# Performance work log

Hardware: AMD Instinct MI355X
Metric: run time of the kernel (lower is better)

Reference implementation:

```python
import jax, jax.numpy as jnp
import numpy as np
import math

B, N, D, H, NBT = 16, 512, 512, 8, 5
HD = D // H
EPS = 1e-5

def _ln(x, g, b):
    mu = jnp.mean(x, axis=-1, keepdims=True)
    var = jnp.mean(jnp.square(x - mu), axis=-1, keepdims=True)
    return (x - mu) * jax.lax.rsqrt(var + EPS) * g + b

def setup_inputs() -> dict:
    key = jax.random.key(0)
    ks = jax.random.split(key, 16)
    s = 0.02
    inp = {
        'x': jax.random.normal(ks[0], (B, N, D), jnp.float32),
        'adj': jax.random.randint(ks[1], (B, N, N), 0, NBT, jnp.int64),
        'mask': (jax.random.uniform(ks[2], (B, N)) > 0.1).astype(jnp.float32),
        'Wq': jax.random.normal(ks[3], (D, D), jnp.float32) * s,
        'bq': jnp.zeros((D,), jnp.float32),
        'Wk': jax.random.normal(ks[4], (D, D), jnp.float32) * s,
        'bk': jnp.zeros((D,), jnp.float32),
        'Wv': jax.random.normal(ks[5], (D, D), jnp.float32) * s,
        'bv': jnp.zeros((D,), jnp.float32),
        'Wo': jax.random.normal(ks[6], (D, D), jnp.float32) * s,
        'bo': jnp.zeros((D,), jnp.float32),
        'edge_bias': jax.random.normal(ks[7], (NBT, H), jnp.float32) * s,
        'W1': jax.random.normal(ks[8], (D, 4 * D), jnp.float32) * s,
        'b1': jnp.zeros((4 * D,), jnp.float32),
        'W2': jax.random.normal(ks[9], (4 * D, D), jnp.float32) * s,
        'b2': jnp.zeros((D,), jnp.float32),
        'g1': jnp.ones((D,), jnp.float32),
        'beta1': jnp.zeros((D,), jnp.float32),
        'g2': jnp.ones((D,), jnp.float32),
        'beta2': jnp.zeros((D,), jnp.float32),
    }
    return inp

def reference(x, adj, mask, Wq, bq, Wk, bk, Wv, bv, Wo, bo, edge_bias,
              W1, b1, W2, b2, g1, beta1, g2, beta2):
    # --- attention block ---
    residual = x
    h = _ln(x, g1, beta1)
    # (B,N,D) -> (B,H,N,HD)
    Q = (h @ Wq + bq).reshape(B, N, H, HD).transpose(0, 2, 1, 3)
    K = (h @ Wk + bk).reshape(B, N, H, HD).transpose(0, 2, 1, 3)
    V = (h @ Wv + bv).reshape(B, N, H, HD).transpose(0, 2, 1, 3)
    attn = jnp.einsum('bhqd,bhkd->bhqk', Q, K) / math.sqrt(HD)
    # per-head edge-type bias: gather (B,N,N,H) -> (B,H,N,N)
    eb = edge_bias[adj].transpose(0, 3, 1, 2)
    attn = attn + eb
    mask_2d = mask[:, None, None, :] * mask[:, None, :, None]  # (B,1,N,N)
    attn = jnp.where(mask_2d == 0, -jnp.inf, attn)
    attn = jax.nn.softmax(attn, axis=-1)
    attn = jnp.nan_to_num(attn, nan=0.0)  # fully-masked rows -> 0
    out = jnp.einsum('bhqk,bhkd->bhqd', attn, V)
    out = out.transpose(0, 2, 1, 3).reshape(B, N, D)
    out = out @ Wo + bo
    x = residual + out  # dropout is identity in eval
    # --- FFN block ---
    residual = x
    h = _ln(x, g2, beta2)
    h = jax.nn.gelu(h @ W1 + b1, approximate=False) @ W2 + b2
    x = residual + h
    return x * mask[:, :, None]
```

## Files before the change

kernel.cpp:

```cpp
#include <hip/hip_runtime.h>
#include <hip/hip_bf16.h>
#include <math.h>
#include <stdint.h>

typedef __hip_bfloat16 bf16;
typedef __bf16 bf16x8 __attribute__((ext_vector_type(8)));
typedef float f32x4 __attribute__((ext_vector_type(4)));

#define MFMA16 __builtin_amdgcn_mfma_f32_16x16x32_bf16

__device__ __forceinline__ void gll16(const void* gsrc, void* ldst) {
  __builtin_amdgcn_global_load_lds(
      (const __attribute__((address_space(1))) unsigned int*)(uintptr_t)gsrc,
      (__attribute__((address_space(3))) unsigned int*)(uintptr_t)ldst,
      16, 0, 0);
}

__global__ __launch_bounds__(256) void pack_adj(const int* __restrict__ adj,
                                                const float* __restrict__ mask,
                                                unsigned char* __restrict__ out) {
  size_t i0 = ((size_t)blockIdx.x * 256 + threadIdx.x) * 16;
  int b = (int)(i0 >> 18);
  int k0 = (int)(i0 & 511);
  const float* mb = mask + b * 512 + k0;
  const int* ap = adj + i0;
  unsigned char o16[16];
#pragma unroll
  for (int j = 0; j < 16; ++j) {
    o16[j] = (unsigned char)(ap[j] | (mb[j] == 0.f ? 0x80 : 0));
  }
  *(uint4*)(out + i0) = *(const uint4*)o16;
}

__global__ __launch_bounds__(256) void transpose_wt6(
    const float* __restrict__ s0, const float* __restrict__ s1,
    const float* __restrict__ s2, const float* __restrict__ s3,
    const float* __restrict__ s4, const float* __restrict__ s5,
    bf16* __restrict__ d0, bf16* __restrict__ d1, bf16* __restrict__ d2,
    bf16* __restrict__ d3, bf16* __restrict__ d4, bf16* __restrict__ d5) {
  __shared__ float t[32][33];
  const int bid = blockIdx.x;
  const float* W;
  bf16* Wt;
  int K, N, n0, k0;
  if (bid < 1024) {
    int mi = bid >> 8, tt = bid & 255;
    W = (mi == 0) ? s0 : (mi == 1) ? s1 : (mi == 2) ? s2 : s3;
    Wt = (mi == 0) ? d0 : (mi == 1) ? d1 : (mi == 2) ? d2 : d3;
    K = 512; N = 512; n0 = (tt & 15) * 32; k0 = (tt >> 4) * 32;
  } else if (bid < 2048) {
    int tt = bid - 1024;
    W = s4; Wt = d4; K = 512; N = 2048;
    n0 = (tt & 63) * 32; k0 = (tt >> 6) * 32;
  } else {
    int tt = bid - 2048;
    W = s5; Wt = d5; K = 2048; N = 512;
    n0 = (tt & 15) * 32; k0 = (tt >> 4) * 32;
  }
  int tx = threadIdx.x, ty = threadIdx.y;
#pragma unroll
  for (int s = 0; s < 32; s += 8) t[ty + s][tx] = W[(size_t)(k0 + ty + s) * N + n0 + tx];
  __syncthreads();
#pragma unroll
  for (int s = 0; s < 32; s += 8) Wt[(size_t)(n0 + ty + s) * K + k0 + tx] = (bf16)t[tx][ty + s];
}

__global__ __launch_bounds__(256) void ln_k(const float* __restrict__ x,
                                            const float* __restrict__ gam,
                                            const float* __restrict__ bet,
                                            bf16* __restrict__ out) {
  int l = threadIdx.x & 63, w = threadIdx.x >> 6;
  size_t row = (size_t)blockIdx.x * 4 + w;
  const float* xr = x + row * 512 + l * 8;
  float4 v0 = *(const float4*)xr;
  float4 v1 = *(const float4*)(xr + 4);
  float s = v0.x + v0.y + v0.z + v0.w + v1.x + v1.y + v1.z + v1.w;
  float q = v0.x * v0.x + v0.y * v0.y + v0.z * v0.z + v0.w * v0.w +
            v1.x * v1.x + v1.y * v1.y + v1.z * v1.z + v1.w * v1.w;
#pragma unroll
  for (int o = 1; o < 64; o <<= 1) { s += __shfl_xor(s, o); q += __shfl_xor(q, o); }
  float mean = s * (1.0f / 512.0f);
  float var = q * (1.0f / 512.0f) - mean * mean;
  float rstd = rsqrtf(var + 1e-5f);
  const float* gr = gam + l * 8;
  const float* br = bet + l * 8;
  float4 ga = *(const float4*)gr, gb = *(const float4*)(gr + 4);
  float4 ba = *(const float4*)br, bb = *(const float4*)(br + 4);
  bf16 t8[8];
  t8[0] = (bf16)((v0.x - mean) * rstd * ga.x + ba.x);
  t8[1] = (bf16)((v0.y - mean) * rstd * ga.y + ba.y);
  t8[2] = (bf16)((v0.z - mean) * rstd * ga.z + ba.z);
  t8[3] = (bf16)((v0.w - mean) * rstd * ga.w + ba.w);
  t8[4] = (bf16)((v1.x - mean) * rstd * gb.x + bb.x);
  t8[5] = (bf16)((v1.y - mean) * rstd * gb.y + bb.y);
  t8[6] = (bf16)((v1.z - mean) * rstd * gb.z + bb.z);
  t8[7] = (bf16)((v1.w - mean) * rstd * gb.w + bb.w);
  *(uint4*)(out + row * 512 + l * 8) = *(const uint4*)t8;
}

template <int MODE, int BM, int BN>
__global__ __launch_bounds__(256) void gemm_bt(
    const bf16* __restrict__ A, const bf16* __restrict__ Bt, int M, int N, int K,
    const float* __restrict__ b0, const float* __restrict__ b1p,
    const float* __restrict__ b2p, const float* __restrict__ resid,
    const float* __restrict__ mrow, float* __restrict__ outF,
    bf16* __restrict__ outH) {
  constexpr int RA = BM / 32, RB = BN / 32;
  __shared__ __align__(16) bf16 Asw[2][BM * 64];
  __shared__ __align__(16) bf16 Bsw[2][BN * 64];
  const int tid = threadIdx.x;
  const int l = tid & 63, w = tid >> 6;
  const int g = l >> 4, ln = l & 15;
  const int wm = w >> 1, wn = w & 1;
  const int m0 = blockIdx.x * BM, n0 = blockIdx.y * BN;

  f32x4 acc[RA][RB];
  f32x4 zero = {0.f, 0.f, 0.f, 0.f};
#pragma unroll
  for (int i = 0; i < RA; ++i)
#pragma unroll
    for (int j = 0; j < RB; ++j) acc[i][j] = zero;

  const bf16* aSrc[RA];
  const bf16* bSrc[RB];
#pragma unroll
  for (int rr = 0; rr < RA; ++rr) {
    int m = w * (BM / 4) + rr * 8 + (l >> 3);
    int gs = (l & 7) ^ (m & 7);
    aSrc[rr] = A + (size_t)(m0 + m) * K + gs * 8;
  }
#pragma unroll
  for (int rr = 0; rr < RB; ++rr) {
    int n = w * (BN / 4) + rr * 8 + (l >> 3);
    int gs = (l & 7) ^ (n & 7);
    bSrc[rr] = Bt + (size_t)(n0 + n) * K + gs * 8;
  }

  const int NT = K >> 6;
#pragma unroll
  for (int rr = 0; rr < RA; ++rr) gll16(aSrc[rr], &Asw[0][w * (BM * 16) + rr * 512]);
#pragma unroll
  for (int rr = 0; rr < RB; ++rr) gll16(bSrc[rr], &Bsw[0][w * (BN * 16) + rr * 512]);
  __syncthreads();

  for (int ti = 0; ti < NT; ++ti) {
    const int cur = ti & 1, nxt = cur ^ 1;
    if (ti + 1 < NT) {
      const int kt = (ti + 1) << 6;
#pragma unroll
      for (int rr = 0; rr < RA; ++rr)
        gll16(aSrc[rr] + kt, &Asw[nxt][w * (BM * 16) + rr * 512]);
#pragma unroll
      for (int rr = 0; rr < RB; ++rr)
        gll16(bSrc[rr] + kt, &Bsw[nxt][w * (BN * 16) + rr * 512]);
    }
#pragma unroll
    for (int kk = 0; kk < 2; ++kk) {
      bf16x8 af[RA], bfr[RB];
#pragma unroll
      for (int mt = 0; mt < RA; ++mt) {
        int m = wm * (BM / 2) + mt * 16 + ln;
        af[mt] = *(const bf16x8*)&Asw[cur][m * 64 + (((kk * 4 + g) ^ (m & 7)) * 8)];
      }
#pragma unroll
      for (int nt = 0; nt < RB; ++nt) {
        int n = wn * (BN / 2) + nt * 16 + ln;
        bfr[nt] = *(const bf16x8*)&Bsw[cur][n * 64 + (((kk * 4 + g) ^ (n & 7)) * 8)];
      }
#pragma unroll
      for (int mt = 0; mt < RA; ++mt)
#pragma unroll
        for (int nt = 0; nt < RB; ++nt)
          acc[mt][nt] = MFMA16(af[mt], bfr[nt], acc[mt][nt], 0, 0, 0);
    }
    __syncthreads();
  }

#pragma unroll
  for (int mt = 0; mt < RA; ++mt) {
#pragma unroll
    for (int nt = 0; nt < RB; ++nt) {
#pragma unroll
      for (int r = 0; r < 4; ++r) {
        int gm = m0 + wm * (BM / 2) + mt * 16 + g * 4 + r;
        int gn = n0 + wn * (BN / 2) + nt * 16 + ln;
        float v = acc[mt][nt][r];
        if (MODE == 0) {
          int which = gn >> 9;
          int dm = gn & 511;
          const float* bb = (which == 0) ? b0 : ((which == 1) ? b1p : b2p);
          v += bb[dm];
          if (which == 0) v *= 0.125f;
          int hh = dm >> 6, hd = dm & 63;
          int bq = gm >> 9, qq = gm & 511;
          outH[(size_t)which * 4194304 + (((size_t)(bq * 8 + hh)) * 512 + qq) * 64 + hd] =
              (bf16)v;
        } else if (MODE == 1) {
          v += b0[gn] + resid[(size_t)gm * 512 + gn];
          outF[(size_t)gm * 512 + gn] = v;
        } else if (MODE == 2) {
          v += b0[gn];
          v = 0.5f * v * (1.0f + erff(v * 0.70710678118f));
          outH[(size_t)gm * 2048 + gn] = (bf16)v;
        } else {
          v += b0[gn] + resid[(size_t)gm * 512 + gn];
          v *= mrow[gm];
          outF[(size_t)gm * 512 + gn] = v;
        }
      }
    }
  }
}

__global__ __launch_bounds__(256, 4) void attn_k(
    const bf16* __restrict__ Qg, const bf16* __restrict__ Kg,
    const bf16* __restrict__ Vg, const unsigned char* __restrict__ adj8,
    const float* __restrict__ mask, const float* __restrict__ ebias,
    bf16* __restrict__ out) {
  __shared__ __align__(16) bf16 Ksw[2][64 * 64];
  __shared__ __align__(16) bf16 Vt[2][64 * 64];
  __shared__ __align__(16) bf16 Pb[4][16 * 64];
  const int tid = threadIdx.x;
  const int l = tid & 63, w = tid >> 6, g = l >> 4, ln = l & 15;
  const int bh = blockIdx.y, b = bh >> 3, h = bh & 7;
  const int qt = blockIdx.x;
  const bf16* kb = Kg + (size_t)bh * 512 * 64;
  const bf16* vb = Vg + (size_t)bh * 512 * 64;

  int ksrc_off[2];
#pragma unroll
  for (int rr = 0; rr < 2; ++rr) {
    int m = w * 16 + rr * 8 + (l >> 3);
    int gs = (l & 7) ^ (l >> 3);
    ksrc_off[rr] = m * 64 + gs * 8;
  }
  int vd0[2];
#pragma unroll
  for (int it = 0; it < 2; ++it) vd0[it] = (it * 4 + w) * 8;

  const int qrow = qt * 64 + w * 16 + ln;
  const bf16* qp = Qg + ((size_t)bh * 512 + qrow) * 64;
  bf16x8 qf0 = *(const bf16x8*)(qp + g * 8);
  bf16x8 qf1 = *(const bf16x8*)(qp + 32 + g * 8);

  const bool rowlive = mask[b * 512 + qrow] != 0.f;
  float e0 = ebias[0 * 8 + h], e1 = ebias[1 * 8 + h], e2 = ebias[2 * 8 + h];
  float e3 = ebias[3 * 8 + h], e4 = ebias[4 * 8 + h];
  const unsigned char* adjq = adj8 + ((size_t)b * 512 + qrow) * 512;

  f32x4 zero = {0.f, 0.f, 0.f, 0.f};
  f32x4 o[4];
#pragma unroll
  for (int dt = 0; dt < 4; ++dt) o[dt] = zero;
  float rsum = 0.f;
  bf16* pw = &Pb[w][0];

#pragma unroll
  for (int rr = 0; rr < 2; ++rr) gll16(kb + ksrc_off[rr], &Ksw[0][w * 1024 + rr * 512]);
#pragma unroll
  for (int it = 0; it < 2; ++it) {
    uint4 v = *(const uint4*)(vb + l * 64 + vd0[it]);
    const bf16* pv = (const bf16*)&v;
#pragma unroll
    for (int j = 0; j < 8; ++j)
      Vt[0][(vd0[it] + j) * 64 + (((l >> 3) ^ j) * 8) + (l & 7)] = pv[j];
  }
  uchar4 c4[4];
#pragma unroll
  for (int t4 = 0; t4 < 4; ++t4) c4[t4] = *(const uchar4*)(adjq + t4 * 16 + g * 4);
  __syncthreads();

  for (int t = 0; t < 8; ++t) {
    const int cur = t & 1, nxt = cur ^ 1;
    uint4 vv[2];
    uchar4 n4[4];
    if (t < 7) {
      const bf16* kbt = kb + (t + 1) * 4096;
#pragma unroll
      for (int rr = 0; rr < 2; ++rr)
        gll16(kbt + ksrc_off[rr], &Ksw[nxt][w * 1024 + rr * 512]);
      const bf16* vbt = vb + (t + 1) * 4096;
#pragma unroll
      for (int it = 0; it < 2; ++it) vv[it] = *(const uint4*)(vbt + l * 64 + vd0[it]);
#pragma unroll
      for (int t4 = 0; t4 < 4; ++t4)
        n4[t4] = *(const uchar4*)(adjq + (t + 1) * 64 + t4 * 16 + g * 4);
    }

    f32x4 s[4];
#pragma unroll
    for (int t4 = 0; t4 < 4; ++t4) {
      int kr = t4 * 16 + ln;
      s[t4] = zero;
      bf16x8 a0 = *(const bf16x8*)&Ksw[cur][kr * 64 + ((g ^ (ln & 7)) * 8)];
      s[t4] = MFMA16(a0, qf0, s[t4], 0, 0, 0);
      bf16x8 a1 = *(const bf16x8*)&Ksw[cur][kr * 64 + (((4 + g) ^ (ln & 7)) * 8)];
      s[t4] = MFMA16(a1, qf1, s[t4], 0, 0, 0);
    }

    if (t < 7) {
#pragma unroll
      for (int it = 0; it < 2; ++it) {
        const bf16* pv = (const bf16*)&vv[it];
#pragma unroll
        for (int j = 0; j < 8; ++j)
          Vt[nxt][(vd0[it] + j) * 64 + (((l >> 3) ^ j) * 8) + (l & 7)] = pv[j];
      }
    }

#pragma unroll
    for (int t4 = 0; t4 < 4; ++t4) {
      unsigned char cv[4] = {c4[t4].x, c4[t4].y, c4[t4].z, c4[t4].w};
      bf16 hb[4];
#pragma unroll
      for (int r = 0; r < 4; ++r) {
        int a = cv[r] & 7;
        float eb = (a == 0) ? e0 : (a == 1) ? e1 : (a == 2) ? e2 : (a == 3) ? e3 : e4;
        float p = (!rowlive || (cv[r] & 0x80)) ? 0.f : __expf(s[t4][r] + eb);
        rsum += p;
        hb[r] = (bf16)p;
      }
      int sub = t4 * 2 + (g >> 1);
      *(uint2*)&pw[ln * 64 + ((sub ^ (ln & 7)) * 8) + (g & 1) * 4] = *(const uint2*)hb;
    }

#pragma unroll
    for (int ks = 0; ks < 2; ++ks) {
      bf16x8 pa = *(const bf16x8*)&pw[ln * 64 + (((ks * 4 + g) ^ (ln & 7)) * 8)];
#pragma unroll
      for (int dt = 0; dt < 4; ++dt) {
        int d = dt * 16 + ln;
        bf16x8 vvv = *(const bf16x8*)&Vt[cur][d * 64 + (((ks * 4 + g) ^ (ln & 7)) * 8)];
        o[dt] = MFMA16(pa, vvv, o[dt], 0, 0, 0);
      }
    }
    __syncthreads();
    if (t < 7) {
#pragma unroll
      for (int t4 = 0; t4 < 4; ++t4) c4[t4] = n4[t4];
    }
  }

  rsum += __shfl_xor(rsum, 16);
  rsum += __shfl_xor(rsum, 32);
  float inv = (rsum > 0.f) ? 1.f / rsum : 0.f;
  const int qbase = qt * 64 + w * 16;
#pragma unroll
  for (int r = 0; r < 4; ++r) {
    float invr = __shfl(inv, g * 4 + r);
#pragma unroll
    for (int dt = 0; dt < 4; ++dt) {
      int q = qbase + g * 4 + r;
      out[((size_t)b * 512 + q) * 512 + h * 64 + dt * 16 + ln] = (bf16)(o[dt][r] * invr);
    }
  }
}

extern "C" void kernel_launch(void* const* d_in, const int* in_sizes, int n_in,
                              void* d_out, int out_size, void* d_ws, size_t ws_size,
                              hipStream_t stream) {
  const float* x = (const float*)d_in[0];
  const int* adj = (const int*)d_in[1];
  const float* mask = (const float*)d_in[2];
  const float* Wq = (const float*)d_in[3];
  const float* bq = (const float*)d_in[4];
  const float* Wk = (const float*)d_in[5];
  const float* bk = (const float*)d_in[6];
  const float* Wv = (const float*)d_in[7];
  const float* bv = (const float*)d_in[8];
  const float* Wo = (const float*)d_in[9];
  const float* bo = (const float*)d_in[10];
  const float* ebias = (const float*)d_in[11];
  const float* W1 = (const float*)d_in[12];
  const float* b1 = (const float*)d_in[13];
  const float* W2 = (const float*)d_in[14];
  const float* b2 = (const float*)d_in[15];
  const float* g1 = (const float*)d_in[16];
  const float* be1 = (const float*)d_in[17];
  const float* g2 = (const float*)d_in[18];
  const float* be2 = (const float*)d_in[19];
  float* outp = (float*)d_out;

  char* ws = (char*)d_ws;
  size_t off = 0;
  auto alloc = [&](size_t bytes) {
    void* p = ws + off;
    off += (bytes + 255) & ~(size_t)255;
    return p;
  };
  const size_t QSZ = 4194304;
  bf16* h1 = (bf16*)alloc(8192UL * 512 * 2);
  bf16* wqkv = (bf16*)alloc(1536UL * 512 * 2);
  bf16* wo_t = (bf16*)alloc(512UL * 512 * 2);
  bf16* w1_t = (bf16*)alloc(2048UL * 512 * 2);
  bf16* w2_t = (bf16*)alloc(512UL * 2048 * 2);
  bf16* qkv = (bf16*)alloc(3UL * QSZ * 2);
  bf16* aout = (bf16*)alloc(8192UL * 512 * 2);
  float* xmid = (float*)alloc(8192UL * 512 * 4);
  bf16* h2 = (bf16*)alloc(8192UL * 512 * 2);
  bf16* a1 = (bf16*)alloc(8192UL * 2048 * 2);
  unsigned char* adj8 = (unsigned char*)alloc(4194304UL);
  if (off > ws_size) return;

  pack_adj<<<1024, 256, 0, stream>>>(adj, mask, adj8);
  transpose_wt6<<<3072, dim3(32, 8), 0, stream>>>(Wq, Wk, Wv, Wo, W1, W2, wqkv,
                                                  wqkv + 512 * 512, wqkv + 1024 * 512,
                                                  wo_t, w1_t, w2_t);

  ln_k<<<2048, 256, 0, stream>>>(x, g1, be1, h1);
  gemm_bt<0, 128, 128><<<dim3(64, 12), 256, 0, stream>>>(
      h1, wqkv, 8192, 1536, 512, bq, bk, bv, nullptr, nullptr, nullptr, qkv);
  attn_k<<<dim3(8, 128), 256, 0, stream>>>(qkv, qkv + QSZ, qkv + 2 * QSZ, adj8, mask,
                                           ebias, aout);
  gemm_bt<1, 64, 64><<<dim3(128, 8), 256, 0, stream>>>(
      aout, wo_t, 8192, 512, 512, bo, nullptr, nullptr, x, nullptr, xmid, nullptr);
  ln_k<<<2048, 256, 0, stream>>>(xmid, g2, be2, h2);
  gemm_bt<2, 128, 128><<<dim3(64, 16), 256, 0, stream>>>(
      h2, w1_t, 8192, 2048, 512, b1, nullptr, nullptr, nullptr, nullptr, nullptr, a1);
  gemm_bt<3, 64, 64><<<dim3(128, 8), 256, 0, stream>>>(
      a1, w2_t, 8192, 512, 2048, b2, nullptr, nullptr, xmid, mask, outp, nullptr);
}
```

Measured before the change: 153.5 us.

## Write V pre-transposed from QKV GEMM and use exp2 in attention

The QKV GEMM epilogue now writes V in a per-head transposed layout (d-major, tokens contiguous) into a separate buffer. The attention kernel can then stage V tiles with async global-to-LDS loads, replacing the per-element LDS scatter transpose done on every iteration. Separately, log2(e) is folded into the Q scale and the edge biases so the softmax uses the hardware exp2 instead of __expf. The V store in the GEMM epilogue becomes 8-byte strided writes, which may coalesce less well than before.

Result: no change. 153.9 us (+0.2%).

```diff
diff --git a/kernel.cpp b/kernel.cpp
--- a/kernel.cpp
+++ b/kernel.cpp
@@ -8,6 +8,7 @@
 typedef float f32x4 __attribute__((ext_vector_type(4)));
 
 #define MFMA16 __builtin_amdgcn_mfma_f32_16x16x32_bf16
+#define L2E 1.4426950408889634f
 
 __device__ __forceinline__ void gll16(const void* gsrc, void* ldst) {
   __builtin_amdgcn_global_load_lds(
@@ -104,7 +105,7 @@
     const float* __restrict__ b0, const float* __restrict__ b1p,
     const float* __restrict__ b2p, const float* __restrict__ resid,
     const float* __restrict__ mrow, float* __restrict__ outF,
-    bf16* __restrict__ outH) {
+    bf16* __restrict__ outH, bf16* __restrict__ outV) {
   constexpr int RA = BM / 32, RB = BN / 32;
   __shared__ __align__(16) bf16 Asw[2][BM * 64];
   __shared__ __align__(16) bf16 Bsw[2][BN * 64];
@@ -180,32 +181,47 @@
   for (int mt = 0; mt < RA; ++mt) {
 #pragma unroll
     for (int nt = 0; nt < RB; ++nt) {
-#pragma unroll
-      for (int r = 0; r < 4; ++r) {
-        int gm = m0 + wm * (BM / 2) + mt * 16 + g * 4 + r;
-        int gn = n0 + wn * (BN / 2) + nt * 16 + ln;
-        float v = acc[mt][nt][r];
-        if (MODE == 0) {
-          int which = gn >> 9;
-          int dm = gn & 511;
-          const float* bb = (which == 0) ? b0 : ((which == 1) ? b1p : b2p);
-          v += bb[dm];
-          if (which == 0) v *= 0.125f;
-          int hh = dm >> 6, hd = dm & 63;
-          int bq = gm >> 9, qq = gm & 511;
-          outH[(size_t)which * 4194304 + (((size_t)(bq * 8 + hh)) * 512 + qq) * 64 + hd] =
-              (bf16)v;
-        } else if (MODE == 1) {
-          v += b0[gn] + resid[(size_t)gm * 512 + gn];
-          outF[(size_t)gm * 512 + gn] = v;
-        } else if (MODE == 2) {
-          v += b0[gn];
-          v = 0.5f * v * (1.0f + erff(v * 0.70710678118f));
-          outH[(size_t)gm * 2048 + gn] = (bf16)v;
+      if (MODE == 0) {
+        const int gn = n0 + wn * (BN / 2) + nt * 16 + ln;
+        const int which = gn >> 9;
+        const int dm = gn & 511;
+        const int hh = dm >> 6, hd = dm & 63;
+        const float bias = (which == 0) ? b0[dm] : ((which == 1) ? b1p[dm] : b2p[dm]);
+        const int gm0 = m0 + wm * (BM / 2) + mt * 16 + g * 4;
+        const int bq = gm0 >> 9, qq0 = gm0 & 511;
+        if (which == 2) {
+          bf16 t4[4];
+#pragma unroll
+          for (int r = 0; r < 4; ++r) t4[r] = (bf16)(acc[mt][nt][r] + bias);
+          *(uint2*)&outV[(((size_t)(bq * 8 + hh)) * 64 + hd) * 512 + qq0] =
+              *(const uint2*)t4;
         } else {
-          v += b0[gn] + resid[(size_t)gm * 512 + gn];
-          v *= mrow[gm];
-          outF[(size_t)gm * 512 + gn] = v;
+#pragma unroll
+          for (int r = 0; r < 4; ++r) {
+            float v = acc[mt][nt][r] + bias;
+            if (which == 0) v *= 0.125f * L2E;
+            outH[(size_t)which * 4194304 + (((size_t)(bq * 8 + hh)) * 512 + qq0 + r) * 64 + hd] =
+                (bf16)v;
+          }
+        }
+      } else {
+#pragma unroll
+        for (int r = 0; r < 4; ++r) {
+          int gm = m0 + wm * (BM / 2) + mt * 16 + g * 4 + r;
+          int gn = n0 + wn * (BN / 2) + nt * 16 + ln;
+          float v = acc[mt][nt][r];
+          if (MODE == 1) {
+            v += b0[gn] + resid[(size_t)gm * 512 + gn];
+            outF[(size_t)gm * 512 + gn] = v;
+          } else if (MODE == 2) {
+            v += b0[gn];
+            v = 0.5f * v * (1.0f + erff(v * 0.70710678118f));
+            outH[(size_t)gm * 2048 + gn] = (bf16)v;
+          } else {
+            v += b0[gn] + resid[(size_t)gm * 512 + gn];
+            v *= mrow[gm];
+            outF[(size_t)gm * 512 + gn] = v;
+          }
         }
       }
     }
@@ -214,7 +230,7 @@
 
 __global__ __launch_bounds__(256, 4) void attn_k(
     const bf16* __restrict__ Qg, const bf16* __restrict__ Kg,
-    const bf16* __restrict__ Vg, const unsigned char* __restrict__ adj8,
+    const bf16* __restrict__ Vtg, const unsigned char* __restrict__ adj8,
     const float* __restrict__ mask, const float* __restrict__ ebias,
     bf16* __restrict__ out) {
   __shared__ __align__(16) bf16 Ksw[2][64 * 64];
@@ -225,18 +241,16 @@
   const int bh = blockIdx.y, b = bh >> 3, h = bh & 7;
   const int qt = blockIdx.x;
   const bf16* kb = Kg + (size_t)bh * 512 * 64;
-  const bf16* vb = Vg + (size_t)bh * 512 * 64;
-
-  int ksrc_off[2];
+  const bf16* vtb = Vtg + (size_t)bh * 64 * 512;
+
+  int ksrc_off[2], vtsrc_off[2];
 #pragma unroll
   for (int rr = 0; rr < 2; ++rr) {
     int m = w * 16 + rr * 8 + (l >> 3);
     int gs = (l & 7) ^ (l >> 3);
     ksrc_off[rr] = m * 64 + gs * 8;
-  }
-  int vd0[2];
-#pragma unroll
-  for (int it = 0; it < 2; ++it) vd0[it] = (it * 4 + w) * 8;
+    vtsrc_off[rr] = m * 512 + gs * 8;
+  }
 
   const int qrow = qt * 64 + w * 16 + ln;
   const bf16* qp = Qg + ((size_t)bh * 512 + qrow) * 64;
@@ -244,8 +258,9 @@
   bf16x8 qf1 = *(const bf16x8*)(qp + 32 + g * 8);
 
   const bool rowlive = mask[b * 512 + qrow] != 0.f;
-  float e0 = ebias[0 * 8 + h], e1 = ebias[1 * 8 + h], e2 = ebias[2 * 8 + h];
-  float e3 = ebias[3 * 8 + h], e4 = ebias[4 * 8 + h];
+  float e0 = ebias[0 * 8 + h] * L2E, e1 = ebias[1 * 8 + h] * L2E;
+  float e2 = ebias[2 * 8 + h] * L2E, e3 = ebias[3 * 8 + h] * L2E;
+  float e4 = ebias[4 * 8 + h] * L2E;
   const unsigned char* adjq = adj8 + ((size_t)b * 512 + qrow) * 512;
 
   f32x4 zero = {0.f, 0.f, 0.f, 0.f};
@@ -256,14 +271,9 @@
   bf16* pw = &Pb[w][0];
 
 #pragma unroll
-  for (int rr = 0; rr < 2; ++rr) gll16(kb + ksrc_off[rr], &Ksw[0][w * 1024 + rr * 512]);
-#pragma unroll
-  for (int it = 0; it < 2; ++it) {
-    uint4 v = *(const uint4*)(vb + l * 64 + vd0[it]);
-    const bf16* pv = (const bf16*)&v;
-#pragma unroll
-    for (int j = 0; j < 8; ++j)
-      Vt[0][(vd0[it] + j) * 64 + (((l >> 3) ^ j) * 8) + (l & 7)] = pv[j];
+  for (int rr = 0; rr < 2; ++rr) {
+    gll16(kb + ksrc_off[rr], &Ksw[0][w * 1024 + rr * 512]);
+    gll16(vtb + vtsrc_off[rr], &Vt[0][w * 1024 + rr * 512]);
   }
   uchar4 c4[4];
 #pragma unroll
@@ -272,16 +282,15 @@
 
   for (int t = 0; t < 8; ++t) {
     const int cur = t & 1, nxt = cur ^ 1;
-    uint4 vv[2];
     uchar4 n4[4];
     if (t < 7) {
       const bf16* kbt = kb + (t + 1) * 4096;
-#pragma unroll
-      for (int rr = 0; rr < 2; ++rr)
+      const bf16* vbt = vtb + (t + 1) * 64;
+#pragma unroll
+      for (int rr = 0; rr < 2; ++rr) {
         gll16(kbt + ksrc_off[rr], &Ksw[nxt][w * 1024 + rr * 512]);
-      const bf16* vbt = vb + (t + 1) * 4096;
-#pragma unroll
-      for (int it = 0; it < 2; ++it) vv[it] = *(const uint4*)(vbt + l * 64 + vd0[it]);
+        gll16(vbt + vtsrc_off[rr], &Vt[nxt][w * 1024 + rr * 512]);
+      }
 #pragma unroll
       for (int t4 = 0; t4 < 4; ++t4)
         n4[t4] = *(const uchar4*)(adjq + (t + 1) * 64 + t4 * 16 + g * 4);
@@ -298,16 +307,6 @@
       s[t4] = MFMA16(a1, qf1, s[t4], 0, 0, 0);
     }
 
-    if (t < 7) {
-#pragma unroll
-      for (int it = 0; it < 2; ++it) {
-        const bf16* pv = (const bf16*)&vv[it];
-#pragma unroll
-        for (int j = 0; j < 8; ++j)
-          Vt[nxt][(vd0[it] + j) * 64 + (((l >> 3) ^ j) * 8) + (l & 7)] = pv[j];
-      }
-    }
-
 #pragma unroll
     for (int t4 = 0; t4 < 4; ++t4) {
       unsigned char cv[4] = {c4[t4].x, c4[t4].y, c4[t4].z, c4[t4].w};
@@ -316,7 +315,9 @@
       for (int r = 0; r < 4; ++r) {
         int a = cv[r] & 7;
         float eb = (a == 0) ? e0 : (a == 1) ? e1 : (a == 2) ? e2 : (a == 3) ? e3 : e4;
-        float p = (!rowlive || (cv[r] & 0x80)) ? 0.f : __expf(s[t4][r] + eb);
+        float p = (!rowlive || (cv[r] & 0x80))
+                      ? 0.f
+                      : __builtin_amdgcn_exp2f(s[t4][r] + eb);
         rsum += p;
         hb[r] = (bf16)p;
       }
@@ -330,7 +331,7 @@
 #pragma unroll
       for (int dt = 0; dt < 4; ++dt) {
         int d = dt * 16 + ln;
-        bf16x8 vvv = *(const bf16x8*)&Vt[cur][d * 64 + (((ks * 4 + g) ^ (ln & 7)) * 8)];
+        bf16x8 vvv = *(const bf16x8*)&Vt[cur][d * 64 + (((ks * 4 + g) ^ (d & 7)) * 8)];
         o[dt] = MFMA16(pa, vvv, o[dt], 0, 0, 0);
       }
     }
@@ -394,7 +395,8 @@
   bf16* wo_t = (bf16*)alloc(512UL * 512 * 2);
   bf16* w1_t = (bf16*)alloc(2048UL * 512 * 2);
   bf16* w2_t = (bf16*)alloc(512UL * 2048 * 2);
-  bf16* qkv = (bf16*)alloc(3UL * QSZ * 2);
+  bf16* qkv = (bf16*)alloc(2UL * QSZ * 2);
+  bf16* vt = (bf16*)alloc(QSZ * 2);
   bf16* aout = (bf16*)alloc(8192UL * 512 * 2);
   float* xmid = (float*)alloc(8192UL * 512 * 4);
   bf16* h2 = (bf16*)alloc(8192UL * 512 * 2);
@@ -409,14 +411,16 @@
 
   ln_k<<<2048, 256, 0, stream>>>(x, g1, be1, h1);
   gemm_bt<0, 128, 128><<<dim3(64, 12), 256, 0, stream>>>(
-      h1, wqkv, 8192, 1536, 512, bq, bk, bv, nullptr, nullptr, nullptr, qkv);
-  attn_k<<<dim3(8, 128), 256, 0, stream>>>(qkv, qkv + QSZ, qkv + 2 * QSZ, adj8, mask,
-                                           ebias, aout);
+      h1, wqkv, 8192, 1536, 512, bq, bk, bv, nullptr, nullptr, nullptr, qkv, vt);
+  attn_k<<<dim3(8, 128), 256, 0, stream>>>(qkv, qkv + QSZ, vt, adj8, mask, ebias, aout);
   gemm_bt<1, 64, 64><<<dim3(128, 8), 256, 0, stream>>>(
-      aout, wo_t, 8192, 512, 512, bo, nullptr, nullptr, x, nullptr, xmid, nullptr);
+      aout, wo_t, 8192, 512, 512, bo, nullptr, nullptr, x, nullptr, xmid, nullptr,
+      nullptr);
   ln_k<<<2048, 256, 0, stream>>>(xmid, g2, be2, h2);
   gemm_bt<2, 128, 128><<<dim3(64, 16), 256, 0, stream>>>(
-      h2, w1_t, 8192, 2048, 512, b1, nullptr, nullptr, nullptr, nullptr, nullptr, a1);
+      h2, w1_t, 8192, 2048, 512, b1, nullptr, nullptr, nullptr, nullptr, nullptr, a1,
+      nullptr);
   gemm_bt<3, 64, 64><<<dim3(128, 8), 256, 0, stream>>>(
-      a1, w2_t, 8192, 512, 2048, b2, nullptr, nullptr, xmid, mask, outp, nullptr);
-}
+      a1, w2_t, 8192, 512, 2048, b2, nullptr, nullptr, xmid, mask, outp, nullptr,
+      nullptr);
+}
```
